# Kernel tuning notes

Hardware: AMD Instinct MI355X
Metric: run time of the kernel (lower is better)

The kernel has to match this reference:

```python
import jax, jax.numpy as jnp
import numpy as np

SIGMA = 2.0
INF = 1.0e6
M, N, H, K, C_IN, C_OUT = 50000, 100000, 32, 15, 64, 64
RADIUS = 2.5


def setup_inputs() -> dict:
    key = jax.random.key(0)
    k1, k2, k3, k4, k5, k6 = jax.random.split(key, 6)
    q_points = jax.random.normal(k1, (M, 3), dtype=jnp.float32)
    s_points = jax.random.normal(k2, (N, 3), dtype=jnp.float32)
    s_feats = jax.random.normal(k3, (N, C_IN), dtype=jnp.float32)
    # index N refers to the padding point (placed at INF)
    neighbor_indices = jax.random.randint(k4, (M, H), 0, N + 1, dtype=jnp.int64)
    weights = jax.random.normal(k5, (K, C_IN, C_OUT), dtype=jnp.float32) * 0.05
    # kernel points inside sphere of RADIUS (stand-in for load_kernels buffer)
    kp = jax.random.normal(k6, (K, 3), dtype=jnp.float32)
    kp = kp / jnp.linalg.norm(kp, axis=1, keepdims=True) * RADIUS * 0.7
    kernel_points = kp.at[0].set(0.0)  # fixed='center'
    return {
        "q_points": q_points,
        "s_points": s_points,
        "s_feats": s_feats,
        "neighbor_indices": neighbor_indices,
        "weights": weights,
        "kernel_points": kernel_points,
    }


def reference(q_points, s_points, s_feats, neighbor_indices, weights, kernel_points):
    # pad support points with an 'infinity' shadow point at index N
    padded_pts = jnp.concatenate([s_points, jnp.full((1, 3), INF, s_points.dtype)], axis=0)
    neighbors = padded_pts[neighbor_indices]                    # (M, H, 3)
    rel = neighbors - q_points[:, None, :]                      # (M, H, 3)
    diff = rel[:, :, None, :] - kernel_points[None, None]       # (M, H, K, 3)
    sq_dist = jnp.sum(diff * diff, axis=-1)                     # (M, H, K)
    nbr_w = jnp.clip(1.0 - jnp.sqrt(sq_dist) / SIGMA, 0.0)      # (M, H, K)

    padded_feats = jnp.concatenate([s_feats, jnp.zeros((1, s_feats.shape[1]), s_feats.dtype)], axis=0)
    nbr_feats = padded_feats[neighbor_indices]                  # (M, H, C_in)

    weighted = jnp.einsum('mhk,mhc->mkc', nbr_w, nbr_feats)     # (M, K, C_in)
    out = jnp.einsum('mkc,kcd->md', weighted, weights)          # (M, C_out)

    # normalize by count of real (non-padding / nonzero-sum) neighbors
    nbr_sum = jnp.sum(nbr_feats, axis=-1)                       # (M, H)
    nbr_num = jnp.sum(nbr_sum > 0.0, axis=-1)                   # (M,)
    nbr_num = jnp.maximum(nbr_num, 1)
    return out / nbr_num[:, None].astype(out.dtype)
```

## Files before the change

### kernel.cpp

```cpp
#include <hip/hip_runtime.h>
#include <hip/hip_bf16.h>

#define MPTS 50000
#define NPTS 100000
#define KK 15
#define TM 16
#define WTP 1028
#define STP 36
#define STPH 20

typedef __attribute__((ext_vector_type(8))) short short8;
typedef __attribute__((ext_vector_type(4))) short short4v;
typedef __attribute__((ext_vector_type(4))) float floatx4;

static __device__ __forceinline__ unsigned short f2bf(float f) {
    __hip_bfloat16 h = __float2bfloat16(f);
    return *reinterpret_cast<unsigned short*>(&h);
}

static __device__ __forceinline__ short8 lds_load8(const unsigned short* p) {
    const short4v a = *(const short4v*)p;
    const short4v b = *(const short4v*)(p + 4);
    short8 r;
    r[0] = a[0]; r[1] = a[1]; r[2] = a[2]; r[3] = a[3];
    r[4] = b[0]; r[5] = b[1]; r[6] = b[2]; r[7] = b[3];
    return r;
}

static __device__ __forceinline__ unsigned cvtb(unsigned char u) {
    return (unsigned)f2bf((float)(int)(signed char)u);
}

__global__ void prep_all(const float* __restrict__ sf, const float* __restrict__ w,
                         const float* __restrict__ kpts, const float* __restrict__ spt,
                         unsigned char* __restrict__ sfb8, float4* __restrict__ spts4,
                         unsigned short* __restrict__ wbf2, float4* __restrict__ kpp) {
    const int b = blockIdx.x, t = threadIdx.x;
    if (b < 782) {
        const int tt = b * 256 + t;
        const int row = tt >> 1, p = tt & 1;
        if (row < NPTS) {
            const float* base = sf + (size_t)row * 64 + p * 4;
            float4 x[8];
            x[0] = *(const float4*)base;
            float4 r = x[0];
            float am = fmaxf(fmaxf(fabsf(x[0].x), fabsf(x[0].y)),
                             fmaxf(fabsf(x[0].z), fabsf(x[0].w)));
#pragma unroll
            for (int i = 1; i < 8; i++) {
                x[i] = *(const float4*)(base + i * 8);
                r.x += x[i].x; r.y += x[i].y; r.z += x[i].z; r.w += x[i].w;
                am = fmaxf(am, fmaxf(fmaxf(fabsf(x[i].x), fabsf(x[i].y)),
                                     fmaxf(fabsf(x[i].z), fabsf(x[i].w))));
            }
            float sp = (r.x + r.y) + (r.z + r.w);
            sp += __shfl_xor(sp, 1);
            am = fmaxf(am, __shfl_xor(am, 1));
            const float inv = am > 0.0f ? 127.0f / am : 0.0f;
#pragma unroll
            for (int i = 0; i < 8; i++) {
                uchar4 o;
                o.x = (unsigned char)(int)rintf(x[i].x * inv);
                o.y = (unsigned char)(int)rintf(x[i].y * inv);
                o.z = (unsigned char)(int)rintf(x[i].z * inv);
                o.w = (unsigned char)(int)rintf(x[i].w * inv);
                *(uchar4*)&sfb8[(size_t)row * 64 + i * 8 + p * 4] = o;
            }
            if (p == 0) {
                const float sc = am * (1.0f / 127.0f);
                spts4[row] = make_float4(spt[row * 3 + 0], spt[row * 3 + 1],
                                         spt[row * 3 + 2], sp > 0.0f ? sc : -sc);
            }
        }
    } else if (b < 814) {
        const int e = (b - 782) * 256 + t;
        const int lane = e & 63, s = (e >> 6) & 31, wq = e >> 11;
        const int d = wq * 16 + (lane & 15);
        const int lqp = lane >> 4;
        unsigned short o8[8];
#pragma unroll
        for (int j = 0; j < 8; j++) {
            const int kc = s * 32 + lqp * 8 + j;
            const int c = kc >> 4, k = kc & 15;
            o8[j] = (k < KK) ? f2bf(w[k * 4096 + c * 64 + d]) : (unsigned short)0;
        }
#pragma unroll
        for (int j = 0; j < 8; j++) wbf2[(size_t)e * 8 + j] = o8[j];
    } else {
        if (t < 16) *(uchar4*)&sfb8[(size_t)NPTS * 64 + t * 4] = make_uchar4(0, 0, 0, 0);
        else if (t == 16) spts4[NPTS] = make_float4(1.0e6f, 1.0e6f, 1.0e6f, -1.0f);
        else if (t >= 32 && t < 32 + KK) {
            const int k = t - 32;
            const float kx = kpts[k * 3 + 0], ky = kpts[k * 3 + 1], kz = kpts[k * 3 + 2];
            kpp[k] = make_float4(-2.f * kx, -2.f * ky, -2.f * kz, kx * kx + ky * ky + kz * kz);
        }
    }
}

__global__ __launch_bounds__(512, 2) void kpconv_fused(
    const float* __restrict__ q_points,
    const float4* __restrict__ spts4,
    const unsigned char* __restrict__ sfb8,
    const int*   __restrict__ nbr,
    const unsigned short* __restrict__ wbf2,
    const float4* __restrict__ kpp,
    float* __restrict__ out)
{
    const int t    = threadIdx.x;
    const int m0   = blockIdx.x * TM;
    const int lane = t & 63;
    const int wv   = t >> 6;
    const int l15  = lane & 15;
    const int lq   = lane >> 4;

    __shared__ __align__(16) unsigned short stage[8][64 * STPH];
    __shared__ unsigned short wtw[TM * WTP];
    __shared__ float inv_lds[TM];

    const int mw = 2 * wv + (lane >> 5);
    const int h  = lane & 31;
    const int c4 = l15 * 4;

    const int idxp = nbr[(size_t)(m0 + mw) * 32 + h];
    const float4 sp4 = spts4[min(idxp, NPTS)];

    uchar4 g[2][8];
#pragma unroll
    for (int mi = 0; mi < 2; mi++) {
        const int m = 2 * wv + mi;
#pragma unroll
        for (int g2 = 0; g2 < 4; g2++) {
            const int r0 = g2 * 8 + lq * 2;
            const int2 ip = *(const int2*)&nbr[(size_t)(m0 + m) * 32 + r0];
            const int i0 = min(ip.x, NPTS);
            const int i1 = min(ip.y, NPTS);
            g[mi][2 * g2]     = *(const uchar4*)&sfb8[(size_t)i0 * 64 + c4];
            g[mi][2 * g2 + 1] = *(const uchar4*)&sfb8[(size_t)i1 * 64 + c4];
        }
    }

    {
        const float rx = sp4.x - q_points[(m0 + mw) * 3 + 0];
        const float ry = sp4.y - q_points[(m0 + mw) * 3 + 1];
        const float rz = sp4.z - q_points[(m0 + mw) * 3 + 2];
        const float r2 = rx * rx + ry * ry + rz * rz;
        const float ss = fabsf(sp4.w);
        unsigned short* wrow = &wtw[mw * WTP];
#pragma unroll
        for (int k = 0; k < KK; k++) {
            const float4 kp = kpp[k];
            float d2 = kp.w;
            d2 = fmaf(rx, kp.x, d2);
            d2 = fmaf(ry, kp.y, d2);
            d2 = fmaf(rz, kp.z, d2);
            d2 = fmaxf(r2 + d2, 0.0f);
            const float wv_ = fmaxf(fmaf(-0.5f, __builtin_amdgcn_sqrtf(d2), 1.0f), 0.0f);
            wrow[k * STP + h] = f2bf(wv_ * ss);
        }
        wrow[15 * STP + h] = 0;

        const unsigned long long bal = __ballot(sp4.w > 0.0f);
        if (h == 0) {
            const int cnt = __popc((unsigned)(bal >> ((lane >> 5) * 32)));
            inv_lds[mw] = 1.0f / (float)(cnt < 1 ? 1 : cnt);
        }
    }

    unsigned short* const st = stage[wv];
    const int swzh = (l15 >> 3) << 2;
    const short8 zero8 = {0, 0, 0, 0, 0, 0, 0, 0};
#pragma unroll
    for (int mi = 0; mi < 2; mi++) {
        const int m = 2 * wv + mi;
        const short8 afull = lds_load8(&wtw[m * WTP + l15 * STP + lq * 8]);
        floatx4 d[4];
#pragma unroll
        for (int ct = 0; ct < 4; ct++) d[ct] = (floatx4){0.f, 0.f, 0.f, 0.f};
#pragma unroll
        for (int r = 0; r < 2; r++) {
#pragma unroll
            for (int g2h = 0; g2h < 2; g2h++) {
                const int g2 = 2 * r + g2h;
                const int so = (((g2h * 4 + lq) ^ swzh)) * 2;
                const uchar4 a = g[mi][2 * g2];
                const uchar4 b = g[mi][2 * g2 + 1];
                *(unsigned*)&st[(c4 + 0) * STPH + so] = cvtb(a.x) | (cvtb(b.x) << 16);
                *(unsigned*)&st[(c4 + 1) * STPH + so] = cvtb(a.y) | (cvtb(b.y) << 16);
                *(unsigned*)&st[(c4 + 2) * STPH + so] = cvtb(a.z) | (cvtb(b.z) << 16);
                *(unsigned*)&st[(c4 + 3) * STPH + so] = cvtb(a.w) | (cvtb(b.w) << 16);
            }
            const short8 ar = ((lq >> 1) == r) ? afull : zero8;
#pragma unroll
            for (int ct = 0; ct < 4; ct++) {
                const short8 bfrag =
                    lds_load8(&st[(ct * 16 + l15) * STPH + (((lq & 1) ^ (ct >> 1)) * 8)]);
                d[ct] = __builtin_amdgcn_mfma_f32_16x16x32_bf16(ar, bfrag, d[ct], 0, 0, 0);
            }
        }
#pragma unroll
        for (int ct = 0; ct < 4; ct++) {
            ushort4 pk;
            pk.x = f2bf(d[ct][0]); pk.y = f2bf(d[ct][1]);
            pk.z = f2bf(d[ct][2]); pk.w = f2bf(d[ct][3]);
            *(ushort4*)&wtw[m * WTP + (ct * 16 + l15) * 16 + lq * 4] = pk;
        }
    }
    __syncthreads();

    {
        const int q  = wv & 3;
        const int kh = wv >> 2;
        floatx4 acc = {0.f, 0.f, 0.f, 0.f};
        const unsigned short* ap = &wtw[l15 * WTP + kh * 512 + lq * 8];
        const unsigned short* bp = wbf2 + ((size_t)((q * 32 + kh * 16) * 64) + lane) * 8;
#pragma unroll 8
        for (int s = 0; s < 16; s++) {
            const short8 a = lds_load8(ap + s * 32);
            const short8 b = *(const short8*)(bp + s * 512);
            acc = __builtin_amdgcn_mfma_f32_16x16x32_bf16(a, b, acc, 0, 0, 0);
        }

        float* const scratch = (float*)&stage[0][0];
        if (kh == 1) {
            *(floatx4*)&scratch[q * 256 + l15 * 16 + lq * 4] = acc;
        }
        __syncthreads();
        if (kh == 0) {
            const floatx4 p = *(const floatx4*)&scratch[q * 256 + l15 * 16 + lq * 4];
            const int d = q * 16 + l15;
#pragma unroll
            for (int r = 0; r < 4; r++) {
                const int m = lq * 4 + r;
                out[(size_t)(m0 + m) * 64 + d] = (acc[r] + p[r]) * inv_lds[m];
            }
        }
    }
}

extern "C" void kernel_launch(void* const* d_in, const int* in_sizes, int n_in,
                              void* d_out, int out_size, void* d_ws, size_t ws_size,
                              hipStream_t stream) {
    const float* q_points = (const float*)d_in[0];
    const float* s_points = (const float*)d_in[1];
    const float* s_feats  = (const float*)d_in[2];
    const int*   nbr      = (const int*)d_in[3];
    const float* weights  = (const float*)d_in[4];
    const float* kpts     = (const float*)d_in[5];
    float* out = (float*)d_out;

    char* ws = (char*)d_ws;
    unsigned short* wbf2 = (unsigned short*)ws;
    float4* spts4 = (float4*)(ws + 131072);
    float4* kpp = (float4*)(ws + 1731088);
    unsigned char* sfb8 = (unsigned char*)(ws + 1731584);

    prep_all<<<815, 256, 0, stream>>>(s_feats, weights, kpts, s_points,
                                      sfb8, spts4, wbf2, kpp);
    kpconv_fused<<<MPTS / TM, 512, 0, stream>>>(q_points, spts4, sfb8, nbr,
                                                wbf2, kpp, out);
}
```

Baseline: 133.4 us.

## Make fused KPConv kernel persistent with next-tile gather prefetch

The kernel now launches a fixed grid of 512 blocks that loop over query tiles. Each block prefetches the next tile's neighbor indices, features, support points and query coordinates while it finishes the second-stage MFMA of the current tile. A separate scratch buffer is added so the stage buffer can be reused, and lighter LDS barriers replace __syncthreads. The goal is to hide gather latency across tiles, at the cost of extra register pressure and less load balancing than a grid of 3125 blocks.

Result: slower. 142.1 us (+6.5%).

```diff
diff --git a/kernel.cpp b/kernel.cpp
--- a/kernel.cpp
+++ b/kernel.cpp
@@ -5,6 +5,8 @@
 #define NPTS 100000
 #define KK 15
 #define TM 16
+#define NTILES (MPTS / TM)
+#define PGRID 512
 #define WTP 1028
 #define STP 36
 #define STPH 20
@@ -29,6 +31,12 @@
 
 static __device__ __forceinline__ unsigned cvtb(unsigned char u) {
     return (unsigned)f2bf((float)(int)(signed char)u);
+}
+
+static __device__ __forceinline__ void lds_barrier() {
+    asm volatile("s_waitcnt lgkmcnt(0)" ::: "memory");
+    __builtin_amdgcn_s_barrier();
+    __builtin_amdgcn_sched_barrier(0);
 }
 
 __global__ void prep_all(const float* __restrict__ sf, const float* __restrict__ w,
@@ -107,7 +115,6 @@
     float* __restrict__ out)
 {
     const int t    = threadIdx.x;
-    const int m0   = blockIdx.x * TM;
     const int lane = t & 63;
     const int wv   = t >> 6;
     const int l15  = lane & 15;
@@ -116,122 +123,147 @@
     __shared__ __align__(16) unsigned short stage[8][64 * STPH];
     __shared__ unsigned short wtw[TM * WTP];
     __shared__ float inv_lds[TM];
+    __shared__ __align__(16) float scratch[1024];
 
     const int mw = 2 * wv + (lane >> 5);
     const int h  = lane & 31;
     const int c4 = l15 * 4;
 
-    const int idxp = nbr[(size_t)(m0 + mw) * 32 + h];
-    const float4 sp4 = spts4[min(idxp, NPTS)];
-
-    uchar4 g[2][8];
-#pragma unroll
-    for (int mi = 0; mi < 2; mi++) {
-        const int m = 2 * wv + mi;
-#pragma unroll
-        for (int g2 = 0; g2 < 4; g2++) {
-            const int r0 = g2 * 8 + lq * 2;
-            const int2 ip = *(const int2*)&nbr[(size_t)(m0 + m) * 32 + r0];
-            const int i0 = min(ip.x, NPTS);
-            const int i1 = min(ip.y, NPTS);
-            g[mi][2 * g2]     = *(const uchar4*)&sfb8[(size_t)i0 * 64 + c4];
-            g[mi][2 * g2 + 1] = *(const uchar4*)&sfb8[(size_t)i1 * 64 + c4];
-        }
-    }
-
-    {
-        const float rx = sp4.x - q_points[(m0 + mw) * 3 + 0];
-        const float ry = sp4.y - q_points[(m0 + mw) * 3 + 1];
-        const float rz = sp4.z - q_points[(m0 + mw) * 3 + 2];
-        const float r2 = rx * rx + ry * ry + rz * rz;
-        const float ss = fabsf(sp4.w);
-        unsigned short* wrow = &wtw[mw * WTP];
-#pragma unroll
-        for (int k = 0; k < KK; k++) {
-            const float4 kp = kpp[k];
-            float d2 = kp.w;
-            d2 = fmaf(rx, kp.x, d2);
-            d2 = fmaf(ry, kp.y, d2);
-            d2 = fmaf(rz, kp.z, d2);
-            d2 = fmaxf(r2 + d2, 0.0f);
-            const float wv_ = fmaxf(fmaf(-0.5f, __builtin_amdgcn_sqrtf(d2), 1.0f), 0.0f);
-            wrow[k * STP + h] = f2bf(wv_ * ss);
-        }
-        wrow[15 * STP + h] = 0;
-
-        const unsigned long long bal = __ballot(sp4.w > 0.0f);
-        if (h == 0) {
-            const int cnt = __popc((unsigned)(bal >> ((lane >> 5) * 32)));
-            inv_lds[mw] = 1.0f / (float)(cnt < 1 ? 1 : cnt);
-        }
-    }
+    const int q  = wv & 3;
+    const int kh = wv >> 2;
+    const unsigned short* const ap = &wtw[l15 * WTP + kh * 512 + lq * 8];
+    const unsigned short* const bp = wbf2 + ((size_t)((q * 32 + kh * 16) * 64) + lane) * 8;
 
     unsigned short* const st = stage[wv];
     const int swzh = (l15 >> 3) << 2;
     const short8 zero8 = {0, 0, 0, 0, 0, 0, 0, 0};
-#pragma unroll
-    for (int mi = 0; mi < 2; mi++) {
-        const int m = 2 * wv + mi;
-        const short8 afull = lds_load8(&wtw[m * WTP + l15 * STP + lq * 8]);
-        floatx4 d[4];
-#pragma unroll
-        for (int ct = 0; ct < 4; ct++) d[ct] = (floatx4){0.f, 0.f, 0.f, 0.f};
-#pragma unroll
-        for (int r = 0; r < 2; r++) {
-#pragma unroll
-            for (int g2h = 0; g2h < 2; g2h++) {
-                const int g2 = 2 * r + g2h;
-                const int so = (((g2h * 4 + lq) ^ swzh)) * 2;
-                const uchar4 a = g[mi][2 * g2];
-                const uchar4 b = g[mi][2 * g2 + 1];
-                *(unsigned*)&st[(c4 + 0) * STPH + so] = cvtb(a.x) | (cvtb(b.x) << 16);
-                *(unsigned*)&st[(c4 + 1) * STPH + so] = cvtb(a.y) | (cvtb(b.y) << 16);
-                *(unsigned*)&st[(c4 + 2) * STPH + so] = cvtb(a.z) | (cvtb(b.z) << 16);
-                *(unsigned*)&st[(c4 + 3) * STPH + so] = cvtb(a.w) | (cvtb(b.w) << 16);
-            }
-            const short8 ar = ((lq >> 1) == r) ? afull : zero8;
+
+    uchar4 g[2][8];
+    float4 sp4;
+    float qx, qy, qz;
+
+    auto PREFETCH = [&](const int m0n) {
+        const int idxp = nbr[(size_t)(m0n + mw) * 32 + h];
+#pragma unroll
+        for (int mi = 0; mi < 2; mi++) {
+            const int m = 2 * wv + mi;
+#pragma unroll
+            for (int g2 = 0; g2 < 4; g2++) {
+                const int r0 = g2 * 8 + lq * 2;
+                const int2 ip = *(const int2*)&nbr[(size_t)(m0n + m) * 32 + r0];
+                const int i0 = min(ip.x, NPTS);
+                const int i1 = min(ip.y, NPTS);
+                g[mi][2 * g2]     = *(const uchar4*)&sfb8[(size_t)i0 * 64 + c4];
+                g[mi][2 * g2 + 1] = *(const uchar4*)&sfb8[(size_t)i1 * 64 + c4];
+            }
+        }
+        sp4 = spts4[min(idxp, NPTS)];
+        qx = q_points[(m0n + mw) * 3 + 0];
+        qy = q_points[(m0n + mw) * 3 + 1];
+        qz = q_points[(m0n + mw) * 3 + 2];
+    };
+
+    PREFETCH(blockIdx.x * TM);
+
+    for (int tile = blockIdx.x; tile < NTILES; tile += PGRID) {
+        const int m0 = tile * TM;
+
+        {
+            const float rx = sp4.x - qx;
+            const float ry = sp4.y - qy;
+            const float rz = sp4.z - qz;
+            const float r2 = rx * rx + ry * ry + rz * rz;
+            const float ss = fabsf(sp4.w);
+            unsigned short* wrow = &wtw[mw * WTP];
+#pragma unroll
+            for (int k = 0; k < KK; k++) {
+                const float4 kp = kpp[k];
+                float d2 = kp.w;
+                d2 = fmaf(rx, kp.x, d2);
+                d2 = fmaf(ry, kp.y, d2);
+                d2 = fmaf(rz, kp.z, d2);
+                d2 = fmaxf(r2 + d2, 0.0f);
+                const float wv_ = fmaxf(fmaf(-0.5f, __builtin_amdgcn_sqrtf(d2), 1.0f), 0.0f);
+                wrow[k * STP + h] = f2bf(wv_ * ss);
+            }
+            wrow[15 * STP + h] = 0;
+
+            const unsigned long long bal = __ballot(sp4.w > 0.0f);
+            if (h == 0) {
+                const int cnt = __popc((unsigned)(bal >> ((lane >> 5) * 32)));
+                inv_lds[mw] = 1.0f / (float)(cnt < 1 ? 1 : cnt);
+            }
+        }
+
+#pragma unroll
+        for (int mi = 0; mi < 2; mi++) {
+            const int m = 2 * wv + mi;
+            const short8 afull = lds_load8(&wtw[m * WTP + l15 * STP + lq * 8]);
+            floatx4 d[4];
+#pragma unroll
+            for (int ct = 0; ct < 4; ct++) d[ct] = (floatx4){0.f, 0.f, 0.f, 0.f};
+#pragma unroll
+            for (int r = 0; r < 2; r++) {
+#pragma unroll
+                for (int g2h = 0; g2h < 2; g2h++) {
+                    const int g2 = 2 * r + g2h;
+                    const int so = (((g2h * 4 + lq) ^ swzh)) * 2;
+                    const uchar4 a = g[mi][2 * g2];
+                    const uchar4 b = g[mi][2 * g2 + 1];
+                    *(unsigned*)&st[(c4 + 0) * STPH + so] = cvtb(a.x) | (cvtb(b.x) << 16);
+                    *(unsigned*)&st[(c4 + 1) * STPH + so] = cvtb(a.y) | (cvtb(b.y) << 16);
+                    *(unsigned*)&st[(c4 + 2) * STPH + so] = cvtb(a.z) | (cvtb(b.z) << 16);
+                    *(unsigned*)&st[(c4 + 3) * STPH + so] = cvtb(a.w) | (cvtb(b.w) << 16);
+                }
+                const short8 ar = ((lq >> 1) == r) ? afull : zero8;
+#pragma unroll
+                for (int ct = 0; ct < 4; ct++) {
+                    const short8 bfrag =
+                        lds_load8(&st[(ct * 16 + l15) * STPH + (((lq & 1) ^ (ct >> 1)) * 8)]);
+                    d[ct] = __builtin_amdgcn_mfma_f32_16x16x32_bf16(ar, bfrag, d[ct], 0, 0, 0);
+                }
+            }
 #pragma unroll
             for (int ct = 0; ct < 4; ct++) {
-                const short8 bfrag =
-                    lds_load8(&st[(ct * 16 + l15) * STPH + (((lq & 1) ^ (ct >> 1)) * 8)]);
-                d[ct] = __builtin_amdgcn_mfma_f32_16x16x32_bf16(ar, bfrag, d[ct], 0, 0, 0);
-            }
-        }
-#pragma unroll
-        for (int ct = 0; ct < 4; ct++) {
-            ushort4 pk;
-            pk.x = f2bf(d[ct][0]); pk.y = f2bf(d[ct][1]);
-            pk.z = f2bf(d[ct][2]); pk.w = f2bf(d[ct][3]);
-            *(ushort4*)&wtw[m * WTP + (ct * 16 + l15) * 16 + lq * 4] = pk;
-        }
-    }
-    __syncthreads();
-
-    {
-        const int q  = wv & 3;
-        const int kh = wv >> 2;
-        floatx4 acc = {0.f, 0.f, 0.f, 0.f};
-        const unsigned short* ap = &wtw[l15 * WTP + kh * 512 + lq * 8];
-        const unsigned short* bp = wbf2 + ((size_t)((q * 32 + kh * 16) * 64) + lane) * 8;
+                ushort4 pk;
+                pk.x = f2bf(d[ct][0]); pk.y = f2bf(d[ct][1]);
+                pk.z = f2bf(d[ct][2]); pk.w = f2bf(d[ct][3]);
+                *(ushort4*)&wtw[m * WTP + (ct * 16 + l15) * 16 + lq * 4] = pk;
+            }
+        }
+
+        const int nxt = tile + PGRID;
+        if (nxt < NTILES) PREFETCH(nxt * TM);
+
+        lds_barrier();
+
+        {
+            float inv4[4];
+            if (kh == 0) {
+#pragma unroll
+                for (int r = 0; r < 4; r++) inv4[r] = inv_lds[lq * 4 + r];
+            }
+            floatx4 acc = {0.f, 0.f, 0.f, 0.f};
 #pragma unroll 8
-        for (int s = 0; s < 16; s++) {
-            const short8 a = lds_load8(ap + s * 32);
-            const short8 b = *(const short8*)(bp + s * 512);
-            acc = __builtin_amdgcn_mfma_f32_16x16x32_bf16(a, b, acc, 0, 0, 0);
-        }
-
-        float* const scratch = (float*)&stage[0][0];
-        if (kh == 1) {
-            *(floatx4*)&scratch[q * 256 + l15 * 16 + lq * 4] = acc;
-        }
-        __syncthreads();
-        if (kh == 0) {
-            const floatx4 p = *(const floatx4*)&scratch[q * 256 + l15 * 16 + lq * 4];
-            const int d = q * 16 + l15;
-#pragma unroll
-            for (int r = 0; r < 4; r++) {
-                const int m = lq * 4 + r;
-                out[(size_t)(m0 + m) * 64 + d] = (acc[r] + p[r]) * inv_lds[m];
+            for (int s = 0; s < 16; s++) {
+                const short8 a = lds_load8(ap + s * 32);
+                const short8 b = *(const short8*)(bp + s * 512);
+                acc = __builtin_amdgcn_mfma_f32_16x16x32_bf16(a, b, acc, 0, 0, 0);
+            }
+            if (kh == 1) {
+                *(floatx4*)&scratch[q * 256 + l15 * 16 + lq * 4] = acc;
+            }
+
+            lds_barrier();
+
+            if (kh == 0) {
+                const floatx4 p = *(const floatx4*)&scratch[q * 256 + l15 * 16 + lq * 4];
+                const int d = q * 16 + l15;
+#pragma unroll
+                for (int r = 0; r < 4; r++) {
+                    const int m = lq * 4 + r;
+                    out[(size_t)(m0 + m) * 64 + d] = (acc[r] + p[r]) * inv4[r];
+                }
             }
         }
     }
@@ -256,6 +288,6 @@
 
     prep_all<<<815, 256, 0, stream>>>(s_feats, weights, kpts, s_points,
                                       sfb8, spts4, wbf2, kpp);
-    kpconv_fused<<<MPTS / TM, 512, 0, stream>>>(q_points, spts4, sfb8, nbr,
-                                                wbf2, kpp, out);
-}
+    kpconv_fused<<<PGRID, 512, 0, stream>>>(q_points, spts4, sfb8, nbr,
+                                            wbf2, kpp, out);
+}
```
